# Optimization experiments

Hardware: AMD Instinct MI355X
Metric: run time of the kernel (lower is better)

The kernel has to match this reference:

```python
import jax, jax.numpy as jnp
import numpy as np

PAIR_KEY_BASE = 20000  # token_max + 1
POS_WEIGHT = 1.0
NEG_WEIGHT = 1.0
EPS = 1e-8


def _isin_sorted(x, sorted_keys):
    # torch.isin equivalent given a sorted 1-D key set
    idx = jnp.searchsorted(sorted_keys, x)
    idx = jnp.clip(idx, 0, sorted_keys.shape[0] - 1)
    return sorted_keys[idx] == x


def setup_inputs() -> dict:
    key = jax.random.key(0)
    k_ids, k_tf, k_act, k_prior, k_u, k_v = jax.random.split(key, 6)
    B, S, D, M = 8, 2048, 64, 200000
    input_ids = jax.random.randint(k_ids, (B, S), 0, PAIR_KEY_BASE, dtype=jnp.int32)
    tf_mask = jax.random.randint(k_tf, (B, S), 0, 2) == 1
    active_gene_mask = jax.random.randint(k_act, (B, S), 0, 2) == 1
    # prior GRN pair keys: src*base + tgt, sorted (duplicates are harmless for isin)
    prior_pair_keys = jnp.sort(jax.random.randint(
        k_prior, (M,), 0, PAIR_KEY_BASE * PAIR_KEY_BASE, dtype=jnp.int32))
    # u, v small positive so u @ v^T lands mostly inside (0, 1) before clamping
    u = jax.random.uniform(k_u, (B, S, D), dtype=jnp.float32) * 0.1
    v = jax.random.uniform(k_v, (B, S, D), dtype=jnp.float32) * 0.1
    return {"input_ids": input_ids, "tf_mask": tf_mask,
            "active_gene_mask": active_gene_mask,
            "prior_pair_keys": prior_pair_keys, "u": u, "v": v}


def reference(input_ids, tf_mask, active_gene_mask, prior_pair_keys, u, v):
    # supervise: TF rows x active-gene cols  [B,S,S]
    supervise = tf_mask[:, :, None] & active_gene_mask[:, None, :]
    # pair keys for every (src, tgt) position pair  [B,S,S]
    pair_keys = input_ids[:, :, None] * PAIR_KEY_BASE + input_ids[:, None, :]
    positive = _isin_sorted(pair_keys, prior_pair_keys) & supervise
    target = positive.astype(jnp.float32)
    # edge probabilities, clamped like torch: [B,S,S]
    edge_prob = jnp.clip(jnp.einsum('bsd,btd->bst', u, v), EPS, 1.0 - EPS)
    # binary cross entropy, reduction='none'
    loss = -(target * jnp.log(edge_prob) + (1.0 - target) * jnp.log1p(-edge_prob))
    weight = target * POS_WEIGHT + (1.0 - target) * NEG_WEIGHT
    # neg_sample_ratio=None -> sampled_mask == supervise_mask
    m = supervise.astype(jnp.float32)
    numer = jnp.sum(loss * weight * m)
    denom = jnp.sum(weight * m)
    return numer / (denom + EPS)
```

## Files before the change

### kernel.cpp

```cpp
#include <hip/hip_runtime.h>
#include <math.h>

#define BB 8
#define SS 2048
#define DD 64
#define PAIR_BASE 20000
#define CEPS 1e-8f
#define NROWS (BB * SS)
#define MAIN_BLOCKS (16 * 16 * BB)
#define PPMAX 1024
#define PREP_BLOCKS (256 + BB + BB + 1)
#define POISON_WORD 0xAAAAAAAAu
#define CANARY_DONE 0x5A5A5A5Au

typedef __bf16 bf16x8 __attribute__((ext_vector_type(8)));
typedef __bf16 bf16x4 __attribute__((ext_vector_type(4)));
typedef float  f32x4  __attribute__((ext_vector_type(4)));

struct Ws {
    int byteMode;
    unsigned int canary;
    int mc[BB];
    int nc[BB];
    float mpart[MAIN_BLOCKS];
    float ppart[PPMAX];
    int cheadR[BB * PAIR_BASE];
    int cnextR[NROWS];
    int cheadC[BB * PAIR_BASE];
    int cnextC[NROWS];
    __bf16 Uc[(size_t)BB * SS * DD];
    __bf16 Vc[(size_t)BB * SS * DD];
};

__device__ __forceinline__ bool read_mask(const void* p, int i, int byteMode) {
    if (byteMode) return ((const unsigned char*)p)[i] != 0;
    return ((const int*)p)[i] != 0;
}

__device__ __forceinline__ int detect_bm(const void* tf_raw, int tid, int* badl) {
    if (tid == 0) *badl = 0;
    __syncthreads();
    if (((const unsigned int*)tf_raw)[tid] > 1u) atomicOr(badl, 1);
    __syncthreads();
    return *badl;
}

__global__ __launch_bounds__(1024) void prep_kernel(
    const int* __restrict__ ids,
    const void* __restrict__ tf_raw,
    const void* __restrict__ act_raw,
    const float* __restrict__ u,
    const float* __restrict__ v,
    Ws* __restrict__ ws)
{
    __shared__ int badl;
    __shared__ int wsum[16], wbase[16], stot;
    __shared__ unsigned short cidx[SS];

    const int blk  = blockIdx.x;
    const int tid  = threadIdx.x;
    const int w    = tid >> 6;
    const int lane = tid & 63;

    if (blk < 256) {
        const int phase = blk >> 7;
        const int b     = (blk >> 4) & 7;
        const int slice = blk & 15;
        const int bm = detect_bm(tf_raw, tid, &badl);
        const unsigned long long below = ((unsigned long long)1 << lane) - 1;

        const void* mraw = phase ? act_raw : tf_raw;
        const int e0 = b * SS + 2 * tid;
        const int m0 = read_mask(mraw, e0,     bm) ? 1 : 0;
        const int m1 = read_mask(mraw, e0 + 1, bm) ? 1 : 0;
        const unsigned long long k0 = __ballot(m0 != 0);
        const unsigned long long k1 = __ballot(m1 != 0);
        const int exclw = __popcll(k0 & below) + __popcll(k1 & below);
        if (lane == 0) wsum[w] = __popcll(k0) + __popcll(k1);
        __syncthreads();
        if (tid == 0) {
            int run = 0;
            #pragma unroll
            for (int k = 0; k < 16; ++k) { wbase[k] = run; run += wsum[k]; }
            stot = run;
        }
        __syncthreads();
        const int excl = wbase[w] + exclw;
        if (m0) cidx[excl]      = (unsigned short)(2 * tid);
        if (m1) cidx[excl + m0] = (unsigned short)(2 * tid + 1);
        __syncthreads();
        const int total = stot;
        if (tid == 0 && slice == 0) {
            if (phase) ws->nc[b] = total; else ws->mc[b] = total;
        }
        const int tpad = (total + 127) & ~127;
        const int rbeg = slice * 128;
        const int rend = min(rbeg + 128, tpad);
        __bf16* dst = (phase ? ws->Vc : ws->Uc) + (size_t)b * SS * DD;
        const float* src = (phase ? v : u) + (size_t)b * SS * DD;
        const int r_off = tid >> 4, c = tid & 15;
        #pragma unroll
        for (int p4 = 0; p4 < 2; ++p4) {
            const int r = rbeg + p4 * 64 + r_off;
            if (r < rend) {
                bf16x4 hv;
                if (r < total) {
                    const float4 f = *(const float4*)(src + (size_t)cidx[r] * DD + c * 4);
                    hv = (bf16x4){ (__bf16)f.x, (__bf16)f.y, (__bf16)f.z, (__bf16)f.w };
                } else {
                    hv = (bf16x4){ (__bf16)0.f, (__bf16)0.f, (__bf16)0.f, (__bf16)0.f };
                }
                *(bf16x4*)(dst + (size_t)r * DD + c * 4) = hv;
            }
        }
    } else if (blk < 256 + BB) {
        const int b = blk - 256;
        const bool poisoned = (ws->canary == POISON_WORD);
        const int bm = detect_bm(tf_raw, tid, &badl);
        int* head = ws->cheadR + b * PAIR_BASE;
        if (!poisoned) {
            for (int i = tid; i < PAIR_BASE; i += 1024) head[i] = -1;
            __syncthreads();
        }
        for (int s = tid; s < SS; s += 1024) {
            if (read_mask(tf_raw, b * SS + s, bm)) {
                const int id = ids[b * SS + s];
                const int old = atomicExch(&head[id], s);
                ws->cnextR[b * SS + s] = old;
            }
        }
    } else if (blk < 256 + 2 * BB) {
        const int b = blk - (256 + BB);
        const bool poisoned = (ws->canary == POISON_WORD);
        const int bm = detect_bm(tf_raw, tid, &badl);
        int* head = ws->cheadC + b * PAIR_BASE;
        if (!poisoned) {
            for (int i = tid; i < PAIR_BASE; i += 1024) head[i] = -1;
            __syncthreads();
        }
        for (int t = tid; t < SS; t += 1024) {
            if (read_mask(act_raw, b * SS + t, bm)) {
                const int id = ids[b * SS + t];
                const int old = atomicExch(&head[id], t);
                ws->cnextC[b * SS + t] = old;
            }
        }
    } else {
        const int bm = detect_bm(tf_raw, tid, &badl);
        if (tid == 0) ws->byteMode = bm;
    }
}

__global__ __launch_bounds__(256) void positives_kernel(
    const int* __restrict__ prior, int M,
    const float* __restrict__ u,
    const float* __restrict__ v,
    Ws* __restrict__ ws)
{
    __shared__ float wsumS[4];
    const int bid  = blockIdx.x;
    const int tid  = threadIdx.x;
    const int w    = tid >> 6;
    const int lane = tid & 63;

    float lsum = 0.f;
    const int i = bid * 256 + tid;
    if (i < M) {
        const int key = prior[i];
        const bool dup = (i > 0) && (prior[i - 1] == key);
        if (!dup) {
            const unsigned int uk  = (unsigned int)key;
            const unsigned int src = uk / PAIR_BASE;
            const unsigned int tgt = uk - src * PAIR_BASE;
            int rh[BB];
            #pragma unroll
            for (int b = 0; b < BB; ++b)
                rh[b] = ws->cheadR[b * PAIR_BASE + (int)src];
            int th[BB];
            #pragma unroll
            for (int b = 0; b < BB; ++b)
                th[b] = (rh[b] >= 0) ? ws->cheadC[b * PAIR_BASE + (int)tgt] : -1;
            #pragma unroll
            for (int b = 0; b < BB; ++b) {
                if (th[b] < 0) continue;
                const int* nxtR = ws->cnextR + b * SS;
                const int* nxtC = ws->cnextC + b * SS;
                for (int r = rh[b]; r >= 0; r = nxtR[r]) {
                    const float* urow = u + (size_t)(b * SS + r) * DD;
                    for (int t = th[b]; t >= 0; t = nxtC[t]) {
                        const float* vrow = v + (size_t)(b * SS + t) * DD;
                        float dot = 0.f;
                        #pragma unroll
                        for (int k2 = 0; k2 < DD; k2 += 4) {
                            float4 a = *(const float4*)(urow + k2);
                            float4 c = *(const float4*)(vrow + k2);
                            dot += (float)(__bf16)a.x * (float)(__bf16)c.x;
                            dot += (float)(__bf16)a.y * (float)(__bf16)c.y;
                            dot += (float)(__bf16)a.z * (float)(__bf16)c.z;
                            dot += (float)(__bf16)a.w * (float)(__bf16)c.w;
                        }
                        float p = fminf(fmaxf(dot, CEPS), 1.0f - CEPS);
                        float q = fminf(fmaxf(1.0f - dot, CEPS), 1.0f - CEPS);
                        lsum += __logf(q) - __logf(p);
                    }
                }
            }
        }
    }

    #pragma unroll
    for (int o = 32; o > 0; o >>= 1)
        lsum += __shfl_down(lsum, o, 64);
    if (lane == 0) wsumS[w] = lsum;
    __syncthreads();
    if (tid == 0)
        ws->ppart[bid] = wsumS[0] + wsumS[1] + wsumS[2] + wsumS[3];
}

__global__ __launch_bounds__(256) void gemm_kernel(
    Ws* __restrict__ ws)
{
    __shared__ __align__(16) __bf16 Ulds[128 * 72];
    __shared__ __align__(16) __bf16 Vlds[128 * 72];
    __shared__ float wsumS[4];

    const int gid  = blockIdx.x;
    const int tid  = threadIdx.x;
    const int w    = tid >> 6;
    const int lane = tid & 63;

    const int b  = gid >> 8;
    const int by = (gid >> 4) & 15;
    const int bx = gid & 15;
    const int s0 = by * 128;
    const int t0 = bx * 128;

    const int mcp = (ws->mc[b] + 127) & ~127;
    const int ncp = (ws->nc[b] + 127) & ~127;
    if (s0 >= mcp || t0 >= ncp) {
        if (tid == 0) ws->mpart[gid] = 0.0f;
        return;
    }

    const __bf16* ub = ws->Uc + (size_t)(b * SS + s0) * DD;
    const __bf16* vb = ws->Vc + (size_t)(b * SS + t0) * DD;
    #pragma unroll
    for (int it = 0; it < 4; ++it) {
        int li = tid + it * 256;
        int r  = li >> 3;
        int c8 = li & 7;
        *(bf16x8*)&Ulds[r * 72 + c8 * 8] = *(const bf16x8*)(ub + r * DD + c8 * 8);
        *(bf16x8*)&Vlds[r * 72 + c8 * 8] = *(const bf16x8*)(vb + r * DD + c8 * 8);
    }
    __syncthreads();

    const int quad = lane >> 4;
    const int l15  = lane & 15;
    const int wm0  = (w >> 1) * 64;
    const int wn0  = (w & 1) * 64;

    f32x4 acc[4][4];
    #pragma unroll
    for (int i = 0; i < 4; ++i)
        #pragma unroll
        for (int j = 0; j < 4; ++j)
            acc[i][j] = (f32x4){0.f, 0.f, 0.f, 0.f};

    #pragma unroll
    for (int kh = 0; kh < 2; ++kh) {
        const int kcol = kh * 32 + quad * 8;
        bf16x8 af[4], bfr[4];
        #pragma unroll
        for (int ti = 0; ti < 4; ++ti)
            af[ti] = *(const bf16x8*)&Ulds[(wm0 + ti * 16 + l15) * 72 + kcol];
        #pragma unroll
        for (int tj = 0; tj < 4; ++tj)
            bfr[tj] = *(const bf16x8*)&Vlds[(wn0 + tj * 16 + l15) * 72 + kcol];
        #pragma unroll
        for (int ti = 0; ti < 4; ++ti)
            #pragma unroll
            for (int tj = 0; tj < 4; ++tj)
                acc[ti][tj] = __builtin_amdgcn_mfma_f32_16x16x32_bf16(
                    af[ti], bfr[tj], acc[ti][tj], 0, 0, 0);
    }

    float lsum = 0.f;
    #pragma unroll
    for (int ti = 0; ti < 4; ++ti)
        #pragma unroll
        for (int r = 0; r < 4; ++r)
            #pragma unroll
            for (int tj = 0; tj < 4; ++tj) {
                float q = 1.0f - acc[ti][tj][r];
                q = fminf(fmaxf(q, CEPS), 1.0f - CEPS);
                lsum += __logf(q);
            }
    lsum = -lsum;

    #pragma unroll
    for (int o = 32; o > 0; o >>= 1)
        lsum += __shfl_down(lsum, o, 64);
    if (lane == 0) wsumS[w] = lsum;
    __syncthreads();
    if (tid == 0)
        ws->mpart[gid] = wsumS[0] + wsumS[1] + wsumS[2] + wsumS[3];
}

__global__ __launch_bounds__(256) void finalize_kernel(Ws* __restrict__ ws,
                                                       int npp,
                                                       float* __restrict__ out) {
    __shared__ double sred[256];
    const int tid = threadIdx.x;
    double s = 0.0;
    for (int i = tid; i < MAIN_BLOCKS; i += 256) s += (double)ws->mpart[i];
    for (int i = tid; i < npp;         i += 256) s += (double)ws->ppart[i];
    sred[tid] = s;
    __syncthreads();
    for (int o = 128; o > 0; o >>= 1) {
        if (tid < o) sred[tid] += sred[tid + o];
        __syncthreads();
    }
    if (tid == 0) {
        double denom = 0.0;
        for (int b = 0; b < BB; ++b)
            denom += (double)ws->mc[b] * (double)ws->nc[b];
        out[0] = (float)(sred[0] / (denom + 1e-8));
        ws->canary = CANARY_DONE;
    }
}

extern "C" void kernel_launch(void* const* d_in, const int* in_sizes, int n_in,
                              void* d_out, int out_size, void* d_ws, size_t ws_size,
                              hipStream_t stream) {
    (void)n_in; (void)out_size; (void)ws_size;
    const int*   ids   = (const int*)d_in[0];
    const void*  tf    = d_in[1];
    const void*  act   = d_in[2];
    const int*   prior = (const int*)d_in[3];
    const int    M     = in_sizes[3];
    const float* u     = (const float*)d_in[4];
    const float* v     = (const float*)d_in[5];
    Ws* ws = (Ws*)d_ws;
    float* out = (float*)d_out;

    int npos = (M + 255) / 256;
    if (npos > PPMAX) npos = PPMAX;

    prep_kernel<<<PREP_BLOCKS, 1024, 0, stream>>>(ids, tf, act, u, v, ws);
    if (npos > 0)
        positives_kernel<<<npos, 256, 0, stream>>>(prior, M, u, v, ws);
    gemm_kernel<<<MAIN_BLOCKS, 256, 0, stream>>>(ws);
    finalize_kernel<<<1, 256, 0, stream>>>(ws, npos, out);
}
```

Before: 106.4 us.

## Merge positives and GEMM kernels into one launch, reuse U tile across four column tiles

Combines the prior-pair positives kernel and the masked GEMM/log-loss kernel into a single launch, with a block-index split between the two roles so they can run concurrently and one launch is saved. Each positives block now handles two 256-key chunks. Each GEMM block now loads its U tile once and loops over four V column tiles, cutting redundant U loads and block count. The cost is less parallelism per block, serialised tiles inside a block, and extra barriers.

```diff
diff --git a/kernel.cpp b/kernel.cpp
--- a/kernel.cpp
+++ b/kernel.cpp
@@ -8,6 +8,7 @@
 #define CEPS 1e-8f
 #define NROWS (BB * SS)
 #define MAIN_BLOCKS (16 * 16 * BB)
+#define GEMM_BLOCKS (16 * 16 * BB / 4)
 #define PPMAX 1024
 #define PREP_BLOCKS (256 + BB + BB + 1)
 #define POISON_WORD 0xAAAAAAAAu
@@ -151,159 +152,173 @@
     }
 }
 
-__global__ __launch_bounds__(256) void positives_kernel(
-    const int* __restrict__ prior, int M,
+__global__ __launch_bounds__(256) void work_kernel(
+    const int* __restrict__ prior, int M, int npos, int pblk,
     const float* __restrict__ u,
     const float* __restrict__ v,
-    Ws* __restrict__ ws)
-{
-    __shared__ float wsumS[4];
-    const int bid  = blockIdx.x;
-    const int tid  = threadIdx.x;
-    const int w    = tid >> 6;
-    const int lane = tid & 63;
-
-    float lsum = 0.f;
-    const int i = bid * 256 + tid;
-    if (i < M) {
-        const int key = prior[i];
-        const bool dup = (i > 0) && (prior[i - 1] == key);
-        if (!dup) {
-            const unsigned int uk  = (unsigned int)key;
-            const unsigned int src = uk / PAIR_BASE;
-            const unsigned int tgt = uk - src * PAIR_BASE;
-            int rh[BB];
-            #pragma unroll
-            for (int b = 0; b < BB; ++b)
-                rh[b] = ws->cheadR[b * PAIR_BASE + (int)src];
-            int th[BB];
-            #pragma unroll
-            for (int b = 0; b < BB; ++b)
-                th[b] = (rh[b] >= 0) ? ws->cheadC[b * PAIR_BASE + (int)tgt] : -1;
-            #pragma unroll
-            for (int b = 0; b < BB; ++b) {
-                if (th[b] < 0) continue;
-                const int* nxtR = ws->cnextR + b * SS;
-                const int* nxtC = ws->cnextC + b * SS;
-                for (int r = rh[b]; r >= 0; r = nxtR[r]) {
-                    const float* urow = u + (size_t)(b * SS + r) * DD;
-                    for (int t = th[b]; t >= 0; t = nxtC[t]) {
-                        const float* vrow = v + (size_t)(b * SS + t) * DD;
-                        float dot = 0.f;
-                        #pragma unroll
-                        for (int k2 = 0; k2 < DD; k2 += 4) {
-                            float4 a = *(const float4*)(urow + k2);
-                            float4 c = *(const float4*)(vrow + k2);
-                            dot += (float)(__bf16)a.x * (float)(__bf16)c.x;
-                            dot += (float)(__bf16)a.y * (float)(__bf16)c.y;
-                            dot += (float)(__bf16)a.z * (float)(__bf16)c.z;
-                            dot += (float)(__bf16)a.w * (float)(__bf16)c.w;
-                        }
-                        float p = fminf(fmaxf(dot, CEPS), 1.0f - CEPS);
-                        float q = fminf(fmaxf(1.0f - dot, CEPS), 1.0f - CEPS);
-                        lsum += __logf(q) - __logf(p);
-                    }
-                }
-            }
-        }
-    }
-
-    #pragma unroll
-    for (int o = 32; o > 0; o >>= 1)
-        lsum += __shfl_down(lsum, o, 64);
-    if (lane == 0) wsumS[w] = lsum;
-    __syncthreads();
-    if (tid == 0)
-        ws->ppart[bid] = wsumS[0] + wsumS[1] + wsumS[2] + wsumS[3];
-}
-
-__global__ __launch_bounds__(256) void gemm_kernel(
     Ws* __restrict__ ws)
 {
     __shared__ __align__(16) __bf16 Ulds[128 * 72];
     __shared__ __align__(16) __bf16 Vlds[128 * 72];
     __shared__ float wsumS[4];
 
-    const int gid  = blockIdx.x;
+    const int bid  = blockIdx.x;
     const int tid  = threadIdx.x;
     const int w    = tid >> 6;
     const int lane = tid & 63;
 
-    const int b  = gid >> 8;
-    const int by = (gid >> 4) & 15;
-    const int bx = gid & 15;
-    const int s0 = by * 128;
-    const int t0 = bx * 128;
-
-    const int mcp = (ws->mc[b] + 127) & ~127;
-    const int ncp = (ws->nc[b] + 127) & ~127;
-    if (s0 >= mcp || t0 >= ncp) {
-        if (tid == 0) ws->mpart[gid] = 0.0f;
-        return;
+    if (bid < pblk) {
+        #pragma unroll 1
+        for (int cc = 0; cc < 2; ++cc) {
+            const int chunk = bid * 2 + cc;
+            if (chunk >= npos) break;
+            float lsum = 0.f;
+            const int i = chunk * 256 + tid;
+            if (i < M) {
+                const int key = prior[i];
+                const bool dup = (i > 0) && (prior[i - 1] == key);
+                if (!dup) {
+                    const unsigned int uk  = (unsigned int)key;
+                    const unsigned int src = uk / PAIR_BASE;
+                    const unsigned int tgt = uk - src * PAIR_BASE;
+                    int rh[BB];
+                    #pragma unroll
+                    for (int b = 0; b < BB; ++b)
+                        rh[b] = ws->cheadR[b * PAIR_BASE + (int)src];
+                    int th[BB];
+                    #pragma unroll
+                    for (int b = 0; b < BB; ++b)
+                        th[b] = (rh[b] >= 0) ? ws->cheadC[b * PAIR_BASE + (int)tgt] : -1;
+                    #pragma unroll
+                    for (int b = 0; b < BB; ++b) {
+                        if (th[b] < 0) continue;
+                        const int* nxtR = ws->cnextR + b * SS;
+                        const int* nxtC = ws->cnextC + b * SS;
+                        for (int r = rh[b]; r >= 0; r = nxtR[r]) {
+                            const float* urow = u + (size_t)(b * SS + r) * DD;
+                            for (int t = th[b]; t >= 0; t = nxtC[t]) {
+                                const float* vrow = v + (size_t)(b * SS + t) * DD;
+                                float dot = 0.f;
+                                #pragma unroll
+                                for (int k2 = 0; k2 < DD; k2 += 4) {
+                                    float4 a = *(const float4*)(urow + k2);
+                                    float4 c = *(const float4*)(vrow + k2);
+                                    dot += (float)(__bf16)a.x * (float)(__bf16)c.x;
+                                    dot += (float)(__bf16)a.y * (float)(__bf16)c.y;
+                                    dot += (float)(__bf16)a.z * (float)(__bf16)c.z;
+                                    dot += (float)(__bf16)a.w * (float)(__bf16)c.w;
+                                }
+                                float p = fminf(fmaxf(dot, CEPS), 1.0f - CEPS);
+                                float q = fminf(fmaxf(1.0f - dot, CEPS), 1.0f - CEPS);
+                                lsum += __logf(q) - __logf(p);
+                            }
+                        }
+                    }
+                }
+            }
+            #pragma unroll
+            for (int o = 32; o > 0; o >>= 1)
+                lsum += __shfl_down(lsum, o, 64);
+            if (lane == 0) wsumS[w] = lsum;
+            __syncthreads();
+            if (tid == 0)
+                ws->ppart[chunk] = wsumS[0] + wsumS[1] + wsumS[2] + wsumS[3];
+            __syncthreads();
+        }
+    } else {
+        const int gid = bid - pblk;
+        const int b   = gid >> 6;
+        const int by  = (gid >> 2) & 15;
+        const int bxg = gid & 3;
+        const int s0  = by * 128;
+
+        const int mcp = (ws->mc[b] + 127) & ~127;
+        const int ncp = (ws->nc[b] + 127) & ~127;
+        const bool rowAct = (s0 < mcp);
+
+        if (rowAct) {
+            const __bf16* ub = ws->Uc + (size_t)(b * SS + s0) * DD;
+            #pragma unroll
+            for (int it = 0; it < 4; ++it) {
+                int li = tid + it * 256;
+                int r  = li >> 3;
+                int c8 = li & 7;
+                *(bf16x8*)&Ulds[r * 72 + c8 * 8] = *(const bf16x8*)(ub + r * DD + c8 * 8);
+            }
+        }
+
+        #pragma unroll 1
+        for (int t = 0; t < 4; ++t) {
+            const int bx = bxg * 4 + t;
+            const int t0 = bx * 128;
+            const int slotid = (b << 8) + (by << 4) + bx;
+            if (!rowAct || t0 >= ncp) {
+                if (tid == 0) ws->mpart[slotid] = 0.0f;
+                continue;
+            }
+            const __bf16* vb = ws->Vc + (size_t)(b * SS + t0) * DD;
+            #pragma unroll
+            for (int it = 0; it < 4; ++it) {
+                int li = tid + it * 256;
+                int r  = li >> 3;
+                int c8 = li & 7;
+                *(bf16x8*)&Vlds[r * 72 + c8 * 8] = *(const bf16x8*)(vb + r * DD + c8 * 8);
+            }
+            __syncthreads();
+
+            const int quad = lane >> 4;
+            const int l15  = lane & 15;
+            const int wm0  = (w >> 1) * 64;
+            const int wn0  = (w & 1) * 64;
+
+            f32x4 acc[4][4];
+            #pragma unroll
+            for (int i = 0; i < 4; ++i)
+                #pragma unroll
+                for (int j = 0; j < 4; ++j)
+                    acc[i][j] = (f32x4){0.f, 0.f, 0.f, 0.f};
+
+            #pragma unroll
+            for (int kh = 0; kh < 2; ++kh) {
+                const int kcol = kh * 32 + quad * 8;
+                bf16x8 af[4], bfr[4];
+                #pragma unroll
+                for (int ti = 0; ti < 4; ++ti)
+                    af[ti] = *(const bf16x8*)&Ulds[(wm0 + ti * 16 + l15) * 72 + kcol];
+                #pragma unroll
+                for (int tj = 0; tj < 4; ++tj)
+                    bfr[tj] = *(const bf16x8*)&Vlds[(wn0 + tj * 16 + l15) * 72 + kcol];
+                #pragma unroll
+                for (int ti = 0; ti < 4; ++ti)
+                    #pragma unroll
+                    for (int tj = 0; tj < 4; ++tj)
+                        acc[ti][tj] = __builtin_amdgcn_mfma_f32_16x16x32_bf16(
+                            af[ti], bfr[tj], acc[ti][tj], 0, 0, 0);
+            }
+
+            float lsum = 0.f;
+            #pragma unroll
+            for (int ti = 0; ti < 4; ++ti)
+                #pragma unroll
+                for (int r = 0; r < 4; ++r)
+                    #pragma unroll
+                    for (int tj = 0; tj < 4; ++tj) {
+                        float q = 1.0f - acc[ti][tj][r];
+                        q = fminf(fmaxf(q, CEPS), 1.0f - CEPS);
+                        lsum += __logf(q);
+                    }
+            lsum = -lsum;
+
+            #pragma unroll
+            for (int o = 32; o > 0; o >>= 1)
+                lsum += __shfl_down(lsum, o, 64);
+            if (lane == 0) wsumS[w] = lsum;
+            __syncthreads();
+            if (tid == 0)
+                ws->mpart[slotid] = wsumS[0] + wsumS[1] + wsumS[2] + wsumS[3];
+            __syncthreads();
+        }
     }
-
-    const __bf16* ub = ws->Uc + (size_t)(b * SS + s0) * DD;
-    const __bf16* vb = ws->Vc + (size_t)(b * SS + t0) * DD;
-    #pragma unroll
-    for (int it = 0; it < 4; ++it) {
-        int li = tid + it * 256;
-        int r  = li >> 3;
-        int c8 = li & 7;
-        *(bf16x8*)&Ulds[r * 72 + c8 * 8] = *(const bf16x8*)(ub + r * DD + c8 * 8);
-        *(bf16x8*)&Vlds[r * 72 + c8 * 8] = *(const bf16x8*)(vb + r * DD + c8 * 8);
-    }
-    __syncthreads();
-
-    const int quad = lane >> 4;
-    const int l15  = lane & 15;
-    const int wm0  = (w >> 1) * 64;
-    const int wn0  = (w & 1) * 64;
-
-    f32x4 acc[4][4];
-    #pragma unroll
-    for (int i = 0; i < 4; ++i)
-        #pragma unroll
-        for (int j = 0; j < 4; ++j)
-            acc[i][j] = (f32x4){0.f, 0.f, 0.f, 0.f};
-
-    #pragma unroll
-    for (int kh = 0; kh < 2; ++kh) {
-        const int kcol = kh * 32 + quad * 8;
-        bf16x8 af[4], bfr[4];
-        #pragma unroll
-        for (int ti = 0; ti < 4; ++ti)
-            af[ti] = *(const bf16x8*)&Ulds[(wm0 + ti * 16 + l15) * 72 + kcol];
-        #pragma unroll
-        for (int tj = 0; tj < 4; ++tj)
-            bfr[tj] = *(const bf16x8*)&Vlds[(wn0 + tj * 16 + l15) * 72 + kcol];
-        #pragma unroll
-        for (int ti = 0; ti < 4; ++ti)
-            #pragma unroll
-            for (int tj = 0; tj < 4; ++tj)
-                acc[ti][tj] = __builtin_amdgcn_mfma_f32_16x16x32_bf16(
-                    af[ti], bfr[tj], acc[ti][tj], 0, 0, 0);
-    }
-
-    float lsum = 0.f;
-    #pragma unroll
-    for (int ti = 0; ti < 4; ++ti)
-        #pragma unroll
-        for (int r = 0; r < 4; ++r)
-            #pragma unroll
-            for (int tj = 0; tj < 4; ++tj) {
-                float q = 1.0f - acc[ti][tj][r];
-                q = fminf(fmaxf(q, CEPS), 1.0f - CEPS);
-                lsum += __logf(q);
-            }
-    lsum = -lsum;
-
-    #pragma unroll
-    for (int o = 32; o > 0; o >>= 1)
-        lsum += __shfl_down(lsum, o, 64);
-    if (lane == 0) wsumS[w] = lsum;
-    __syncthreads();
-    if (tid == 0)
-        ws->mpart[gid] = wsumS[0] + wsumS[1] + wsumS[2] + wsumS[3];
 }
 
 __global__ __launch_bounds__(256) void finalize_kernel(Ws* __restrict__ ws,
@@ -345,10 +360,9 @@
 
     int npos = (M + 255) / 256;
     if (npos > PPMAX) npos = PPMAX;
+    const int pblk = (npos + 1) / 2;
 
     prep_kernel<<<PREP_BLOCKS, 1024, 0, stream>>>(ids, tf, act, u, v, ws);
-    if (npos > 0)
-        positives_kernel<<<npos, 256, 0, stream>>>(prior, M, u, v, ws);
-    gemm_kernel<<<MAIN_BLOCKS, 256, 0, stream>>>(ws);
+    work_kernel<<<pblk + GEMM_BLOCKS, 256, 0, stream>>>(prior, M, npos, pblk, u, v, ws);
     finalize_kernel<<<1, 256, 0, stream>>>(ws, npos, out);
 }
```

Measured after the change: 110.8 us. 1.04x slower.
